# Kernel tuning notes

Hardware: AMD Instinct MI355X
Metric: run time of the kernel (lower is better)

## Reference

```python
import jax, jax.numpy as jnp
import numpy as np

B, S, D, H = 4, 2048, 1024, 16
HD = D // H  # head_dim = 64


def setup_inputs() -> dict:
    key = jax.random.key(0)
    ks = jax.random.split(key, 5)
    s = 1.0 / np.sqrt(D)
    return {
        "x": jax.random.normal(ks[0], (B, S, D), jnp.float32),
        "Wq": jax.random.normal(ks[1], (D, D), jnp.float32) * s,
        "Wk": jax.random.normal(ks[2], (D, D), jnp.float32) * s,
        "Wv": jax.random.normal(ks[3], (D, D), jnp.float32) * s,
        "Wo": jax.random.normal(ks[4], (D, D), jnp.float32) * s,
        "bo": jnp.zeros((D,), jnp.float32),
    }


def reference(x, Wq, Wk, Wv, Wo, bo):
    b, s, d = x.shape
    # projections (torch Linear: x @ W.T; weights here stored as [in, out] equivalent)
    q = (x @ Wq).reshape(b, s, H, HD).transpose(0, 2, 1, 3)  # [b,h,s,hd]
    k = (x @ Wk).reshape(b, s, H, HD).transpose(0, 2, 1, 3)
    v = (x @ Wv).reshape(b, s, H, HD).transpose(0, 2, 1, 3)
    scores = jnp.einsum("bhqd,bhkd->bhqk", q, k) * (HD ** -0.5)
    causal = jnp.tril(jnp.ones((s, s), bool))  # mask==0 -> -inf
    scores = jnp.where(causal, scores, -jnp.inf)
    attn = jax.nn.softmax(scores, axis=-1)
    out = jnp.einsum("bhqk,bhkd->bhqd", attn, v)
    out = out.transpose(0, 2, 1, 3).reshape(b, s, d)
    return out @ Wo + bo
```

## Files before the change

kernel.cpp:

```cpp
#include <hip/hip_runtime.h>
#include <cstdint>
#include <cstddef>

typedef __attribute__((ext_vector_type(8))) short bf16x8;
typedef __attribute__((ext_vector_type(4))) short bf16x4;
typedef __attribute__((ext_vector_type(4))) float f32x4;

constexpr int Bsz = 4, Ssz = 2048, Dsz = 1024, Hn = 16, HDsz = 64;
constexpr int Msz = Bsz * Ssz;
constexpr float LOG2E = 1.4426950408889634f;

#define MFMA16(a, b, c) __builtin_amdgcn_mfma_f32_16x16x16bf16_1k(a, b, c, 0, 0, 0)

__device__ __forceinline__ unsigned short f2bf(float f) {
  union { float f; unsigned int u; } v; v.f = f;
  unsigned int r = v.u + 0x7fffu + ((v.u >> 16) & 1u);
  return (unsigned short)(r >> 16);
}

typedef __attribute__((address_space(1))) const unsigned int gu32;
typedef __attribute__((address_space(3))) unsigned int lu32;
__device__ __forceinline__ void async_cp16(const unsigned short* g, unsigned short* l) {
  __builtin_amdgcn_global_load_lds((gu32*)g, (lu32*)l, 16, 0, 0);
}

__global__ void cvt_bf16_kernel(const float* __restrict__ in,
                                unsigned short* __restrict__ out, int n4) {
  int i = blockIdx.x * blockDim.x + threadIdx.x;
  if (i >= n4) return;
  const float4 v = reinterpret_cast<const float4*>(in)[i];
  ushort4 o;
  o.x = f2bf(v.x); o.y = f2bf(v.y); o.z = f2bf(v.z); o.w = f2bf(v.w);
  reinterpret_cast<ushort4*>(out)[i] = o;
}

__global__ void cvt_transpose4_kernel(const float* __restrict__ W0, const float* __restrict__ W1,
                                      const float* __restrict__ W2, const float* __restrict__ W3,
                                      unsigned short* __restrict__ T0, unsigned short* __restrict__ T1,
                                      unsigned short* __restrict__ T2, unsigned short* __restrict__ T3) {
  __shared__ float tile[32][33];
  const int z = blockIdx.z;
  const float* W = (z == 0) ? W0 : (z == 1) ? W1 : (z == 2) ? W2 : W3;
  unsigned short* Wt = (z == 0) ? T0 : (z == 1) ? T1 : (z == 2) ? T2 : T3;
  int tx = threadIdx.x & 31, ty = threadIdx.x >> 5;
  int bx = blockIdx.x, by = blockIdx.y;
#pragma unroll
  for (int i = 0; i < 4; i++) {
    int k = by * 32 + ty + i * 8;
    tile[ty + i * 8][tx] = W[k * Dsz + bx * 32 + tx];
  }
  __syncthreads();
#pragma unroll
  for (int i = 0; i < 4; i++) {
    int nrow = bx * 32 + ty + i * 8;
    Wt[nrow * Dsz + by * 32 + tx] = f2bf(tile[tx][ty + i * 8]);
  }
}

enum { EPI_QKV = 0, EPI_OUT = 1 };

template <int EPI>
__global__ __launch_bounds__(512, 4)
void gemm_bk64(const unsigned short* __restrict__ A,
               const unsigned short* __restrict__ Bt,
               unsigned short* __restrict__ Qh,
               unsigned short* __restrict__ Kh,
               unsigned short* __restrict__ Vth,
               float* __restrict__ Out,
               const float* __restrict__ bias) {
  __shared__ unsigned short As[128 * 64];
  __shared__ unsigned short Bs[128 * 64];

  const int tid = threadIdx.x;
  const int w = tid >> 6, lane = tid & 63;
  const int l15 = lane & 15, quad = lane >> 4;
  const int wr = w >> 1, wc = w & 1;
  const int bm = blockIdx.y, bn = blockIdx.x;
  const int rr = lane >> 3;
  const int scoff = ((lane & 7) ^ rr) * 8;

  f32x4 acc[2][4];
#pragma unroll
  for (int i = 0; i < 2; i++)
#pragma unroll
    for (int j = 0; j < 4; j++) acc[i][j] = (f32x4){0.f, 0.f, 0.f, 0.f};

  const int rowA0 = bm * 128, rowB0 = bn * 128;

  for (int kt = 0; kt < Dsz / 64; kt++) {
#pragma unroll
    for (int i = 0; i < 2; i++) {
      const int r8 = w * 16 + i * 8;
      async_cp16(&A[(size_t)(rowA0 + r8 + rr) * Dsz + kt * 64 + scoff], &As[r8 * 64]);
      async_cp16(&Bt[(size_t)(rowB0 + r8 + rr) * Dsz + kt * 64 + scoff], &Bs[r8 * 64]);
    }
    __syncthreads();

#pragma unroll
    for (int ks = 0; ks < 2; ks++) {
      bf16x8 af[2], bfr[4];
#pragma unroll
      for (int t = 0; t < 2; t++) {
        const int ra = wr * 32 + t * 16 + l15;
        af[t] = *reinterpret_cast<const bf16x8*>(
            &As[ra * 64 + (((ks * 4 + quad) ^ (ra & 7)) * 8)]);
      }
#pragma unroll
      for (int t = 0; t < 4; t++) {
        const int rb = wc * 64 + t * 16 + l15;
        bfr[t] = *reinterpret_cast<const bf16x8*>(
            &Bs[rb * 64 + (((ks * 4 + quad) ^ (rb & 7)) * 8)]);
      }
#pragma unroll
      for (int i = 0; i < 2; i++)
#pragma unroll
        for (int j = 0; j < 4; j++)
          acc[i][j] = __builtin_amdgcn_mfma_f32_16x16x32_bf16(af[i], bfr[j], acc[i][j], 0, 0, 0);
    }
    __syncthreads();
  }

  if (EPI == EPI_QKV) {
    const int proj = (bn * 128) >> 10;
#pragma unroll
    for (int i = 0; i < 2; i++) {
#pragma unroll
      for (int j = 0; j < 4; j++) {
        const int n = bn * 128 + wc * 64 + j * 16 + l15;
        const int nn = n & 1023, h = nn >> 6, hd = nn & 63;
        const int m0 = bm * 128 + wr * 32 + i * 16 + quad * 4;
        const int b = m0 >> 11, s0 = m0 & (Ssz - 1);
        if (proj == 0) {
#pragma unroll
          for (int r = 0; r < 4; r++)
            Qh[((size_t)(b * Hn + h) * Ssz + s0 + r) * HDsz + hd] =
                f2bf(acc[i][j][r] * (0.125f * LOG2E));
        } else if (proj == 1) {
#pragma unroll
          for (int r = 0; r < 4; r++)
            Kh[((size_t)(b * Hn + h) * Ssz + s0 + r) * HDsz + hd] = f2bf(acc[i][j][r]);
        } else {
          ushort4 o;
          o.x = f2bf(acc[i][j][0]); o.y = f2bf(acc[i][j][1]);
          o.z = f2bf(acc[i][j][2]); o.w = f2bf(acc[i][j][3]);
          *reinterpret_cast<ushort4*>(
              &Vth[((size_t)(b * Hn + h) * HDsz + hd) * Ssz + s0]) = o;
        }
      }
    }
  } else {
#pragma unroll
    for (int i = 0; i < 2; i++) {
#pragma unroll
      for (int j = 0; j < 4; j++) {
        const int n = bn * 128 + wc * 64 + j * 16 + l15;
        const int m0 = bm * 128 + wr * 32 + i * 16 + quad * 4;
#pragma unroll
        for (int r = 0; r < 4; r++)
          Out[(size_t)(m0 + r) * Dsz + n] = acc[i][j][r] + bias[n];
      }
    }
  }
}

__global__ __launch_bounds__(256, 4)
void flash_kernel(const unsigned short* __restrict__ Q,
                  const unsigned short* __restrict__ Kg,
                  const unsigned short* __restrict__ Vt,
                  unsigned short* __restrict__ AO) {
  __shared__ unsigned short Ks[64 * 64];
  __shared__ unsigned short Vs[64 * 64];

  const int tid = threadIdx.x;
  const int w = tid >> 6, lane = tid & 63;
  const int l15 = lane & 15, quad = lane >> 4;
  const int rr = lane >> 3;
  const int scoff = ((lane & 7) ^ rr) * 8;

  const int linear = blockIdx.y * 16 + blockIdx.x;
  const int bh = (linear & 7) * 8 + ((linear >> 3) & 7);
  const int t = 15 - (linear >> 6);

  const unsigned short* Qb = Q + (size_t)bh * Ssz * HDsz;
  const unsigned short* Kb = Kg + (size_t)bh * Ssz * HDsz;
  const unsigned short* Vb = Vt + (size_t)bh * HDsz * Ssz;
  const int b = bh / Hn, h = bh % Hn;

  const int q0 = t * 128;
  const int rowStart = q0 + w * 32;

  bf16x8 qf[2][2];
#pragma unroll
  for (int tm = 0; tm < 2; tm++)
#pragma unroll
    for (int ks = 0; ks < 2; ks++)
      qf[tm][ks] = *reinterpret_cast<const bf16x8*>(
          &Qb[(size_t)(rowStart + tm * 16 + l15) * HDsz + ks * 32 + quad * 8]);

  f32x4 oacc[2][4];
  float lpart[2] = {0.f, 0.f};
#pragma unroll
  for (int tm = 0; tm < 2; tm++)
#pragma unroll
    for (int tn = 0; tn < 4; tn++) oacc[tm][tn] = (f32x4){0.f, 0.f, 0.f, 0.f};

  const int nkb = 2 * t + 2;
  for (int kb = 0; kb < nkb; kb++) {
    const int kv0 = kb * 64;
#pragma unroll
    for (int i = 0; i < 2; i++) {
      const int r8 = w * 16 + i * 8;
      async_cp16(&Kb[(size_t)(kv0 + r8 + rr) * HDsz + scoff], &Ks[r8 * 64]);
      async_cp16(&Vb[(size_t)(r8 + rr) * Ssz + kv0 + scoff], &Vs[r8 * 64]);
    }
    __syncthreads();

    const bool skip = (kv0 >= rowStart + 32);
    if (!skip) {
      f32x4 sc[4][2];
#pragma unroll
      for (int tn = 0; tn < 4; tn++)
#pragma unroll
        for (int tm = 0; tm < 2; tm++) sc[tn][tm] = (f32x4){0.f, 0.f, 0.f, 0.f};
#pragma unroll
      for (int ks = 0; ks < 2; ks++) {
#pragma unroll
        for (int tn = 0; tn < 4; tn++) {
          const int rk = tn * 16 + l15;
          bf16x8 kf = *reinterpret_cast<const bf16x8*>(
              &Ks[rk * 64 + (((ks * 4 + quad) ^ (rk & 7)) * 8)]);
#pragma unroll
          for (int tm = 0; tm < 2; tm++)
            sc[tn][tm] = __builtin_amdgcn_mfma_f32_16x16x32_bf16(kf, qf[tm][ks], sc[tn][tm], 0, 0, 0);
        }
      }

      const bool needMask = (kv0 + 63 > rowStart);
      if (needMask) {
#pragma unroll
        for (int tn = 0; tn < 4; tn++)
#pragma unroll
          for (int tm = 0; tm < 2; tm++) {
            const int qrow = rowStart + tm * 16 + l15;
#pragma unroll
            for (int r = 0; r < 4; r++)
              if (kv0 + tn * 16 + quad * 4 + r > qrow) sc[tn][tm][r] = -1e30f;
          }
      }

      unsigned int pk[4][2][2];
#pragma unroll
      for (int tn = 0; tn < 4; tn++)
#pragma unroll
        for (int tm = 0; tm < 2; tm++) {
          union { float f; unsigned int u; } e0, e1, e2, e3;
          e0.f = __builtin_amdgcn_exp2f(sc[tn][tm][0]);
          e1.f = __builtin_amdgcn_exp2f(sc[tn][tm][1]);
          e2.f = __builtin_amdgcn_exp2f(sc[tn][tm][2]);
          e3.f = __builtin_amdgcn_exp2f(sc[tn][tm][3]);
          lpart[tm] += (e0.f + e1.f) + (e2.f + e3.f);
          pk[tn][tm][0] = __builtin_amdgcn_perm(e1.u, e0.u, 0x07060302u);
          pk[tn][tm][1] = __builtin_amdgcn_perm(e3.u, e2.u, 0x07060302u);
        }

#pragma unroll
      for (int tn = 0; tn < 4; tn++) {
        bf16x4 pa[2];
#pragma unroll
        for (int tm = 0; tm < 2; tm++) {
          union { unsigned int u[2]; bf16x4 v; } cv;
          cv.u[0] = pk[tn][tm][0]; cv.u[1] = pk[tn][tm][1];
          pa[tm] = cv.v;
        }
#pragma unroll
        for (int to = 0; to < 4; to++) {
          const int rv = to * 16 + l15;
          const int chunk = tn * 2 + (quad >> 1);
          bf16x4 vf = *reinterpret_cast<const bf16x4*>(
              (const char*)Vs + rv * 128 + ((chunk ^ (rv & 7)) * 16) + (quad & 1) * 8);
#pragma unroll
          for (int tm = 0; tm < 2; tm++)
            oacc[tm][to] = MFMA16(pa[tm], vf, oacc[tm][to]);
        }
      }
    }
    __syncthreads();
  }

#pragma unroll
  for (int tm = 0; tm < 2; tm++) {
    float lf = lpart[tm];
    lf += __shfl_xor(lf, 16);
    lf += __shfl_xor(lf, 32);
    float linv[4];
#pragma unroll
    for (int r = 0; r < 4; r++) {
      union { float f; int i; } cv;
      cv.f = lf;
      cv.i = __builtin_amdgcn_ds_bpermute((quad * 4 + r) * 4, cv.i);
      linv[r] = 1.f / cv.f;
    }
#pragma unroll
    for (int r = 0; r < 4; r++) {
      const int s = rowStart + tm * 16 + quad * 4 + r;
      const size_t m = (size_t)b * Ssz + s;
#pragma unroll
      for (int tn = 0; tn < 4; tn++) {
        const int n = h * HDsz + tn * 16 + l15;
        AO[m * Dsz + n] = f2bf(oacc[tm][tn][r] * linv[r]);
      }
    }
  }
}

extern "C" void kernel_launch(void* const* d_in, const int* in_sizes, int n_in,
                              void* d_out, int out_size, void* d_ws, size_t ws_size,
                              hipStream_t stream) {
  const float* x  = (const float*)d_in[0];
  const float* Wq = (const float*)d_in[1];
  const float* Wk = (const float*)d_in[2];
  const float* Wv = (const float*)d_in[3];
  const float* Wo = (const float*)d_in[4];
  const float* bo = (const float*)d_in[5];
  float* out = (float*)d_out;

  unsigned short* xb  = (unsigned short*)d_ws;
  unsigned short* Wqt = xb + (size_t)Msz * Dsz;
  unsigned short* Wkt = Wqt + (size_t)Dsz * Dsz;
  unsigned short* Wvt = Wkt + (size_t)Dsz * Dsz;
  unsigned short* Wot = Wvt + (size_t)Dsz * Dsz;
  unsigned short* Qh  = Wot + (size_t)Dsz * Dsz;
  unsigned short* Kh  = Qh + (size_t)Msz * Dsz;
  unsigned short* Vth = Kh + (size_t)Msz * Dsz;
  unsigned short* AO  = Vth + (size_t)Msz * Dsz;

  cvt_bf16_kernel<<<(Msz * Dsz / 4 + 255) / 256, 256, 0, stream>>>(x, xb, Msz * Dsz / 4);
  cvt_transpose4_kernel<<<dim3(Dsz / 32, Dsz / 32, 4), 256, 0, stream>>>(
      Wq, Wk, Wv, Wo, Wqt, Wkt, Wvt, Wot);

  gemm_bk64<EPI_QKV><<<dim3(3 * Dsz / 128, Msz / 128), 512, 0, stream>>>(
      xb, Wqt, Qh, Kh, Vth, nullptr, nullptr);

  flash_kernel<<<dim3(16, Bsz * Hn), 256, 0, stream>>>(Qh, Kh, Vth, AO);

  gemm_bk64<EPI_OUT><<<dim3(Dsz / 128, Msz / 128), 512, 0, stream>>>(
      AO, Wot, nullptr, nullptr, nullptr, out, bo);
}
```

Before: 234.5 us.

## Merge prep kernels, rebalance causal tile order, and change LDS swizzle

Fuses the x-to-bf16 conversion and the four weight transpose-conversions into one prep launch, using z-slice 4 for x with 8 float4 per thread. Changes the flash kernel's causal tile schedule so that heavy and light query tiles are interleaved rather than strictly descending. Also modifies the LDS XOR swizzle for K/V so the 16-row MFMA reads use a row-half-dependent pattern, aiming to reduce bank conflicts. This saves one launch and improves load balance, with some risk of the new swizzle mismatching between the store and read sides.

```diff
diff --git a/kernel.cpp b/kernel.cpp
--- a/kernel.cpp
+++ b/kernel.cpp
@@ -24,22 +24,25 @@
   __builtin_amdgcn_global_load_lds((gu32*)g, (lu32*)l, 16, 0, 0);
 }
 
-__global__ void cvt_bf16_kernel(const float* __restrict__ in,
-                                unsigned short* __restrict__ out, int n4) {
-  int i = blockIdx.x * blockDim.x + threadIdx.x;
-  if (i >= n4) return;
-  const float4 v = reinterpret_cast<const float4*>(in)[i];
-  ushort4 o;
-  o.x = f2bf(v.x); o.y = f2bf(v.y); o.z = f2bf(v.z); o.w = f2bf(v.w);
-  reinterpret_cast<ushort4*>(out)[i] = o;
-}
-
-__global__ void cvt_transpose4_kernel(const float* __restrict__ W0, const float* __restrict__ W1,
-                                      const float* __restrict__ W2, const float* __restrict__ W3,
-                                      unsigned short* __restrict__ T0, unsigned short* __restrict__ T1,
-                                      unsigned short* __restrict__ T2, unsigned short* __restrict__ T3) {
+__global__ void prep_kernel(const float* __restrict__ x, unsigned short* __restrict__ xb,
+                            const float* __restrict__ W0, const float* __restrict__ W1,
+                            const float* __restrict__ W2, const float* __restrict__ W3,
+                            unsigned short* __restrict__ T0, unsigned short* __restrict__ T1,
+                            unsigned short* __restrict__ T2, unsigned short* __restrict__ T3) {
+  const int z = blockIdx.z;
+  if (z == 4) {
+    const int i0 = (blockIdx.y * 32 + blockIdx.x) * 2048 + threadIdx.x;
+#pragma unroll
+    for (int j = 0; j < 8; j++) {
+      const int i = i0 + j * 256;
+      const float4 v = reinterpret_cast<const float4*>(x)[i];
+      ushort4 o;
+      o.x = f2bf(v.x); o.y = f2bf(v.y); o.z = f2bf(v.z); o.w = f2bf(v.w);
+      reinterpret_cast<ushort4*>(xb)[i] = o;
+    }
+    return;
+  }
   __shared__ float tile[32][33];
-  const int z = blockIdx.z;
   const float* W = (z == 0) ? W0 : (z == 1) ? W1 : (z == 2) ? W2 : W3;
   unsigned short* Wt = (z == 0) ? T0 : (z == 1) ? T1 : (z == 2) ? T2 : T3;
   int tx = threadIdx.x & 31, ty = threadIdx.x >> 5;
@@ -175,17 +178,19 @@
   const int w = tid >> 6, lane = tid & 63;
   const int l15 = lane & 15, quad = lane >> 4;
   const int rr = lane >> 3;
-  const int scoff = ((lane & 7) ^ rr) * 8;
 
   const int linear = blockIdx.y * 16 + blockIdx.x;
   const int bh = (linear & 7) * 8 + ((linear >> 3) & 7);
-  const int t = 15 - (linear >> 6);
+  const int g = linear >> 6, gk = g >> 2, ga = g & 3;
+  const int t = (gk == 0) ? 15 - ga : (gk == 1) ? 8 + ga : (gk == 2) ? 7 - ga : ga;
 
   const unsigned short* Qb = Q + (size_t)bh * Ssz * HDsz;
   const unsigned short* Kb = Kg + (size_t)bh * Ssz * HDsz;
   const unsigned short* Vb = Vt + (size_t)bh * HDsz * Ssz;
   const int b = bh / Hn, h = bh % Hn;
 
+  const int hl = (l15 & 7) ^ ((l15 >> 3) << 2);
+
   const int q0 = t * 128;
   const int rowStart = q0 + w * 32;
 
@@ -210,8 +215,9 @@
 #pragma unroll
     for (int i = 0; i < 2; i++) {
       const int r8 = w * 16 + i * 8;
-      async_cp16(&Kb[(size_t)(kv0 + r8 + rr) * HDsz + scoff], &Ks[r8 * 64]);
-      async_cp16(&Vb[(size_t)(r8 + rr) * Ssz + kv0 + scoff], &Vs[r8 * 64]);
+      const int sc = (((lane & 7) ^ rr ^ (i << 2))) * 8;
+      async_cp16(&Kb[(size_t)(kv0 + r8 + rr) * HDsz + sc], &Ks[r8 * 64]);
+      async_cp16(&Vb[(size_t)(r8 + rr) * Ssz + kv0 + sc], &Vs[r8 * 64]);
     }
     __syncthreads();
 
@@ -228,7 +234,7 @@
         for (int tn = 0; tn < 4; tn++) {
           const int rk = tn * 16 + l15;
           bf16x8 kf = *reinterpret_cast<const bf16x8*>(
-              &Ks[rk * 64 + (((ks * 4 + quad) ^ (rk & 7)) * 8)]);
+              &Ks[rk * 64 + (((ks * 4 + quad) ^ hl) * 8)]);
 #pragma unroll
           for (int tm = 0; tm < 2; tm++)
             sc[tn][tm] = __builtin_amdgcn_mfma_f32_16x16x32_bf16(kf, qf[tm][ks], sc[tn][tm], 0, 0, 0);
@@ -277,7 +283,7 @@
           const int rv = to * 16 + l15;
           const int chunk = tn * 2 + (quad >> 1);
           bf16x4 vf = *reinterpret_cast<const bf16x4*>(
-              (const char*)Vs + rv * 128 + ((chunk ^ (rv & 7)) * 16) + (quad & 1) * 8);
+              (const char*)Vs + rv * 128 + ((chunk ^ hl) * 16) + (quad & 1) * 8);
 #pragma unroll
           for (int tm = 0; tm < 2; tm++)
             oacc[tm][to] = MFMA16(pa[tm], vf, oacc[tm][to]);
@@ -334,9 +340,8 @@
   unsigned short* Vth = Kh + (size_t)Msz * Dsz;
   unsigned short* AO  = Vth + (size_t)Msz * Dsz;
 
-  cvt_bf16_kernel<<<(Msz * Dsz / 4 + 255) / 256, 256, 0, stream>>>(x, xb, Msz * Dsz / 4);
-  cvt_transpose4_kernel<<<dim3(Dsz / 32, Dsz / 32, 4), 256, 0, stream>>>(
-      Wq, Wk, Wv, Wo, Wqt, Wkt, Wvt, Wot);
+  prep_kernel<<<dim3(32, 32, 5), 256, 0, stream>>>(
+      x, xb, Wq, Wk, Wv, Wo, Wqt, Wkt, Wvt, Wot);
 
   gemm_bk64<EPI_QKV><<<dim3(3 * Dsz / 128, Msz / 128), 512, 0, stream>>>(
       xb, Wqt, Qh, Kh, Vth, nullptr, nullptr);
```

Result: no change. 234.0 us (-0.2%).
